# Performance work log

Measured on AMD Instinct MI355X. Metric: run time of the kernel, lower is better.

Reference implementation:

```python
import jax, jax.numpy as jnp
import numpy as np
from jax import lax

B, T_IN, T_AR = 512, 200, 200
H = 128
L = 2    # num_layers


def setup_inputs() -> dict:
    key = jax.random.key(0)
    k = jax.random.split(key, 8)
    s = 1.0 / np.sqrt(H)
    x = jax.random.normal(k[0], (B, T_IN, H), jnp.float32)
    lengths_in = jax.random.randint(k[1], (B,), T_IN // 2, T_IN + 1).astype(jnp.int32).at[0].set(T_IN)
    lengths_aureg = jax.random.randint(k[2], (B,), T_AR // 2, T_AR + 1).astype(jnp.int32).at[0].set(T_AR)
    mask_aureg = jnp.arange(T_AR)[None, :] < lengths_aureg[:, None]  # [B, T_ar] prefix mask
    W_ih = jax.random.uniform(k[3], (L, 4 * H, H), jnp.float32, -s, s)
    W_hh = jax.random.uniform(k[4], (L, 4 * H, H), jnp.float32, -s, s)
    b_ih = jax.random.uniform(k[5], (L, 4 * H), jnp.float32, -s, s)
    b_hh = jax.random.uniform(k[6], (L, 4 * H), jnp.float32, -s, s)
    return {"x": x, "lengths_in": lengths_in, "lengths_aureg": lengths_aureg,
            "mask_aureg": mask_aureg, "W_ih": W_ih, "W_hh": W_hh, "b_ih": b_ih, "b_hh": b_hh}


def _forward(x, lengths_in, mask_aureg, W_ih, W_hh, b_ih, b_hh):
    def cell_stack(x_t, h, c):
        # one LSTM time step through all layers. x_t: [B,H]; h,c: [L,B,H]
        inp = x_t
        hs, cs = [], []
        for l in range(L):
            z = inp @ W_ih[l].T + h[l] @ W_hh[l].T + (b_ih[l] + b_hh[l])
            i, f, g, o = jnp.split(z, 4, axis=-1)  # PyTorch gate order i,f,g,o
            c_new = jax.nn.sigmoid(f) * c[l] + jax.nn.sigmoid(i) * jnp.tanh(g)
            h_new = jax.nn.sigmoid(o) * jnp.tanh(c_new)
            hs.append(h_new)
            cs.append(c_new)
            inp = h_new
        return jnp.stack(hs), jnp.stack(cs)

    T_in = x.shape[1]
    mask_in = jnp.arange(T_in)[None, :] < lengths_in[:, None]  # [B, T_in]
    h0 = jnp.zeros((L, B, H), x.dtype)

    # Teacher-forcing pass == packed-sequence LSTM: states only advance where t < length,
    # padded output positions are zero (as pad_packed_sequence produces).
    def tf_step(carry, xs):
        h, c = carry
        x_t, m_t = xs  # [B,H], [B]
        h_new, c_new = cell_stack(x_t, h, c)
        m3 = m_t[None, :, None]
        h = jnp.where(m3, h_new, h)
        c = jnp.where(m3, c_new, c)
        out = jnp.where(m_t[:, None], h_new[-1], 0.0)
        return (h, c), out

    (h, c), outs_tf = lax.scan(tf_step, (h0, h0), (x.transpose(1, 0, 2), mask_in.T))
    outputs_teafo = outs_tf.transpose(1, 0, 2)  # [B, T_in, H]

    # input_aureg_init: last-layer hidden at each sequence's final real step
    x_init = h[-1]  # [B, H]

    def ar_step(carry, m_t):
        h, c, xp = carry
        h_new, c_new = cell_stack(xp, h, c)
        m3 = m_t[None, :, None]
        h = jnp.where(m3, h_new, h)
        c = jnp.where(m3, c_new, c)
        out = jnp.where(m_t[:, None], h_new[-1], 0.0)  # temp_output (zeros for inactive rows)
        return (h, c, out), out

    _, outs_ar = lax.scan(ar_step, (h, c, x_init), mask_aureg.T)
    outputs_aureg = outs_ar.transpose(1, 0, 2)  # [B, T_ar, H]
    return outputs_teafo, outputs_aureg


def reference(x, lengths_in, lengths_aureg, mask_aureg, W_ih, W_hh, b_ih, b_hh):
    return _forward(x, lengths_in, mask_aureg, W_ih, W_hh, b_ih, b_hh)
```

## Files before the change

### kernel.cpp

```cpp
#include <hip/hip_runtime.h>
#include <hip/hip_fp16.h>

typedef _Float16 half8 __attribute__((ext_vector_type(8)));
typedef _Float16 half4v __attribute__((ext_vector_type(4)));
typedef float f32x4 __attribute__((ext_vector_type(4)));

#define T_INS 200

constexpr int WI0O = 0;
constexpr int H0O  = 131072;
constexpr int H1O  = 139264;
constexpr int XTO  = 147456;
constexpr int BIO  = 155648;
constexpr int SMSZ = 159744;

#define OFF(b, k) (((((b) << 8) | ((k) << 1))) ^ (((b) & 7) << 4))

#define BARRIER() asm volatile("s_waitcnt lgkmcnt(0)\n\ts_barrier" ::: "memory")

__device__ __forceinline__ float sigm(float x) {
  return __builtin_amdgcn_rcpf(1.0f + __builtin_amdgcn_exp2f(-1.44269504f * x));
}
__device__ __forceinline__ float tanh_f(float x) {
  return 1.0f - 2.0f * __builtin_amdgcn_rcpf(1.0f + __builtin_amdgcn_exp2f(2.88539008f * x));
}
__device__ __forceinline__ half8 cvt_frag(const float* __restrict__ src) {
  f32x4 a = *(const f32x4*)src;
  f32x4 b = *(const f32x4*)(src + 4);
  half8 h;
  h[0] = (_Float16)a[0]; h[1] = (_Float16)a[1]; h[2] = (_Float16)a[2]; h[3] = (_Float16)a[3];
  h[4] = (_Float16)b[0]; h[5] = (_Float16)b[1]; h[6] = (_Float16)b[2]; h[7] = (_Float16)b[3];
  return h;
}
__device__ __forceinline__ int perm_row8(int w, int mt, int r) {
  return (r & 3) * 128 + w * 16 + (r >> 2) * 4 + mt;
}

__global__ __launch_bounds__(256) void pack_kernel(const float* __restrict__ W_ih,
                                                   const float* __restrict__ W_hh,
                                                   char* __restrict__ ws) {
  int gid = blockIdx.x * 256 + threadIdx.x;
  int G = gid >> 6, lane = gid & 63;
  int region = G >> 7, F = G & 127;
  int w = F >> 4, mt = (F >> 2) & 3, kf = F & 3;
  int row = perm_row8(w, mt, lane & 15);
  int k0 = kf * 32 + (lane >> 4) * 8;
  const float* src = (region == 0)
                         ? (W_ih + (size_t)(512 + row) * 128 + k0)
                         : (W_hh + (size_t)((region - 1) * 512 + row) * 128 + k0);
  *(half8*)(ws + (size_t)G * 1024 + lane * 16) = cvt_frag(src);
}

template <int PACKED>
__global__ __launch_bounds__(512, 2) void lstm_kernel(
    const float* __restrict__ x, const int* __restrict__ len_in,
    const int* __restrict__ len_ar, const float* __restrict__ W_ih,
    const float* __restrict__ W_hh, const float* __restrict__ b_ih,
    const float* __restrict__ b_hh, const char* __restrict__ ws,
    float* __restrict__ out) {
  __shared__ __attribute__((aligned(16))) char sm[SMSZ];
  float* biasS = (float*)(sm + BIO);

  const int tid = threadIdx.x;
  const int w = tid >> 6, lane = tid & 63;
  const int lb = lane & 15, lg = lane >> 4;
  const int k0b = lg * 8;
  const int u0 = w * 16 + lg * 4;
  const int batch = blockIdx.x * 16 + lb;
  const int Lin = len_in[batch];
  const int Lar = len_ar[batch];

  for (int j = 0; j < 16; ++j) {
    int pos = tid * 256 + j * 16;
    int F = pos >> 10, ln = (pos >> 4) & 63;
    int fw = F >> 4, fmt = (F >> 2) & 3, fkf = F & 3;
    int row = perm_row8(fw, fmt, ln & 15);
    int k0 = fkf * 32 + (ln >> 4) * 8;
    *(half8*)(sm + WI0O + pos) = cvt_frag(W_ih + (size_t)row * 128 + k0);
  }
  for (int i = tid; i < 1024; i += 512) {
    int l = i >> 9, rp = i & 511, u = rp >> 2, q = rp & 3;
    biasS[i] = b_ih[l * 512 + q * 128 + u] + b_hh[l * 512 + q * 128 + u];
  }
#pragma unroll
  for (int i = 0; i < 2; ++i)
    *(f32x4*)(sm + H0O + tid * 16 + i * 8192) = (f32x4){0.f, 0.f, 0.f, 0.f};
  const int xb = tid >> 5, xk4 = (tid & 31) * 4;
  {
    f32x4 v = *(const f32x4*)(x + ((size_t)(blockIdx.x * 16 + xb) * T_INS) * 128 + xk4);
    half4v hx;
    hx[0] = (_Float16)v[0]; hx[1] = (_Float16)v[1];
    hx[2] = (_Float16)v[2]; hx[3] = (_Float16)v[3];
    *(half4v*)(sm + XTO + OFF(xb, xk4)) = hx;
  }

  half8 whh0[4][4], whh1[4][4], wi1[4][4];
  if (PACKED) {
    const char* base = ws + (size_t)lane * 16;
#pragma unroll
    for (int mt = 0; mt < 4; ++mt)
#pragma unroll
      for (int kf = 0; kf < 4; ++kf) {
        int fo = (w * 16 + mt * 4 + kf) * 1024;
        wi1[mt][kf]  = *(const half8*)(base + fo);
        whh0[mt][kf] = *(const half8*)(base + 131072 + fo);
        whh1[mt][kf] = *(const half8*)(base + 262144 + fo);
      }
  } else {
#pragma unroll
    for (int mt = 0; mt < 4; ++mt)
#pragma unroll
      for (int kf = 0; kf < 4; ++kf) {
        int row = perm_row8(w, mt, lb);
        wi1[mt][kf]  = cvt_frag(W_ih + (size_t)(512 + row) * 128 + kf * 32 + k0b);
        whh0[mt][kf] = cvt_frag(W_hh + (size_t)row * 128 + kf * 32 + k0b);
        whh1[mt][kf] = cvt_frag(W_hh + (size_t)(512 + row) * 128 + kf * 32 + k0b);
      }
  }

  float c0[4], c1[4];
  half4v hp0v, hp1v;
#pragma unroll
  for (int i = 0; i < 4; ++i) {
    c0[i] = c1[i] = 0.f;
    hp0v[i] = (_Float16)0.f; hp1v[i] = (_Float16)0.f;
  }
  __syncthreads();

  const float* xptr = x + ((size_t)(blockIdx.x * 16 + xb) * T_INS + 1) * 128 + xk4;
  float* optr = out + (size_t)batch * 25600 + u0;
  const size_t obase_ar = 13107200ull + (size_t)batch * 25600 + u0;
  const char* wi0base = sm + WI0O + w * 16384 + lane * 16;

  for (int t = 0; t < 400; ++t) {
    const int p = t & 1;
    const bool doX = (t < 199);
    f32x4 xpre = (f32x4){0.f, 0.f, 0.f, 0.f};
    if (doX) { xpre = *(const f32x4*)xptr; xptr += 128; }
    const bool mk = (t < 200) ? (t < Lin) : ((t - 200) < Lar);

    f32x4 acc[4];
    {
      const char* sX = (t < 200) ? (sm + XTO + p * 4096) : (sm + H1O + p * 4096);
      const char* sH = sm + H0O + (p ^ 1) * 4096;
      half8 bf[4];
#pragma unroll
      for (int mt = 0; mt < 4; ++mt)
        acc[mt] = *(const f32x4*)(biasS + (u0 + mt) * 4);
#pragma unroll
      for (int kf = 0; kf < 4; ++kf)
        bf[kf] = *(const half8*)(sH + OFF(lb, kf * 32 + k0b));
#pragma unroll
      for (int kf = 0; kf < 4; ++kf)
#pragma unroll
        for (int mt = 0; mt < 4; ++mt)
          acc[mt] = __builtin_amdgcn_mfma_f32_16x16x32_f16(whh0[mt][kf], bf[kf],
                                                           acc[mt], 0, 0, 0);
#pragma unroll
      for (int kf = 0; kf < 4; ++kf)
        bf[kf] = *(const half8*)(sX + OFF(lb, kf * 32 + k0b));
#pragma unroll
      for (int kf = 0; kf < 4; ++kf)
#pragma unroll
        for (int mt = 0; mt < 4; ++mt) {
          half8 a = *(const half8*)(wi0base + (mt * 4 + kf) * 1024);
          acc[mt] = __builtin_amdgcn_mfma_f32_16x16x32_f16(a, bf[kf], acc[mt], 0, 0, 0);
        }
    }
    {
      _Float16 h4[4];
#pragma unroll
      for (int mt = 0; mt < 4; ++mt) {
        float si = sigm(acc[mt][0]);
        float sf = sigm(acc[mt][1]);
        float tg = tanh_f(acc[mt][2]);
        float so = sigm(acc[mt][3]);
        float cn = sf * c0[mt] + si * tg;
        float hn = so * tanh_f(cn);
        c0[mt] = mk ? cn : c0[mt];
        h4[mt] = (_Float16)hn;
      }
      hp0v = mk ? *(half4v*)h4 : hp0v;
      *(half4v*)(sm + H0O + p * 4096 + OFF(lb, u0)) = hp0v;
    }
    BARRIER();

    if (doX) {
      half4v hx;
      hx[0] = (_Float16)xpre[0]; hx[1] = (_Float16)xpre[1];
      hx[2] = (_Float16)xpre[2]; hx[3] = (_Float16)xpre[3];
      *(half4v*)(sm + XTO + (p ^ 1) * 4096 + OFF(xb, xk4)) = hx;
    }

    {
      const char* sX = sm + H0O + p * 4096;
      const char* sH = sm + H1O + p * 4096;
      half8 bf[4];
#pragma unroll
      for (int mt = 0; mt < 4; ++mt)
        acc[mt] = *(const f32x4*)(biasS + 512 + (u0 + mt) * 4);
#pragma unroll
      for (int kf = 0; kf < 4; ++kf)
        bf[kf] = *(const half8*)(sH + OFF(lb, kf * 32 + k0b));
#pragma unroll
      for (int kf = 0; kf < 4; ++kf)
#pragma unroll
        for (int mt = 0; mt < 4; ++mt)
          acc[mt] = __builtin_amdgcn_mfma_f32_16x16x32_f16(whh1[mt][kf], bf[kf],
                                                           acc[mt], 0, 0, 0);
#pragma unroll
      for (int kf = 0; kf < 4; ++kf)
        bf[kf] = *(const half8*)(sX + OFF(lb, kf * 32 + k0b));
#pragma unroll
      for (int kf = 0; kf < 4; ++kf)
#pragma unroll
        for (int mt = 0; mt < 4; ++mt)
          acc[mt] = __builtin_amdgcn_mfma_f32_16x16x32_f16(wi1[mt][kf], bf[kf],
                                                           acc[mt], 0, 0, 0);
    }
    {
      _Float16 h4[4];
      f32x4 vo;
#pragma unroll
      for (int mt = 0; mt < 4; ++mt) {
        float si = sigm(acc[mt][0]);
        float sf = sigm(acc[mt][1]);
        float tg = tanh_f(acc[mt][2]);
        float so = sigm(acc[mt][3]);
        float cn = sf * c1[mt] + si * tg;
        float hn = so * tanh_f(cn);
        c1[mt] = mk ? cn : c1[mt];
        h4[mt] = (_Float16)hn;
        vo[mt] = mk ? hn : 0.0f;
      }
      hp1v = mk ? *(half4v*)h4 : hp1v;
      *(half4v*)(sm + H1O + (p ^ 1) * 4096 + OFF(lb, u0)) = hp1v;
      *(f32x4*)optr = vo;
      optr += 128;
      if (t == 199) optr = out + obase_ar;
    }
    BARRIER();
  }
}

extern "C" void kernel_launch(void* const* d_in, const int* in_sizes, int n_in,
                              void* d_out, int out_size, void* d_ws, size_t ws_size,
                              hipStream_t stream) {
  (void)in_sizes; (void)n_in; (void)out_size;
  const float* x = (const float*)d_in[0];
  const int* len_in = (const int*)d_in[1];
  const int* len_ar = (const int*)d_in[2];
  const float* W_ih = (const float*)d_in[4];
  const float* W_hh = (const float*)d_in[5];
  const float* b_ih = (const float*)d_in[6];
  const float* b_hh = (const float*)d_in[7];
  float* out = (float*)d_out;
  char* ws = (char*)d_ws;

  if (ws_size >= (size_t)393216) {
    pack_kernel<<<dim3(96), dim3(256), 0, stream>>>(W_ih, W_hh, ws);
    lstm_kernel<1><<<dim3(32), dim3(512), 0, stream>>>(x, len_in, len_ar, W_ih,
                                                       W_hh, b_ih, b_hh, ws, out);
  } else {
    lstm_kernel<0><<<dim3(32), dim3(512), 0, stream>>>(x, len_in, len_ar, W_ih,
                                                       W_hh, b_ih, b_hh, ws, out);
  }
}
```

Baseline: 1.139 ms.

## Hoist layer-0 input projection into a parallel pre-GEMM and prefetch across barriers

Adds a zgemm kernel that computes the layer-0 input projection plus biases for all teacher-forcing timesteps in parallel and stores it to workspace. The recurrent kernel then loads these precomputed gate pre-activations instead of running the x-side MFMAs in the serial loop. The next operands (h fragments, bias, z values) are also issued before each barrier, with partial lgkmcnt waits and sched barriers, to overlap loads with the barrier. This needs about 200 MB of workspace and adds a global-memory load on the critical path at each step. If the workspace is too small it falls back to the old path.

```diff
diff --git a/kernel.cpp b/kernel.cpp
--- a/kernel.cpp
+++ b/kernel.cpp
@@ -14,9 +14,14 @@
 constexpr int BIO  = 155648;
 constexpr int SMSZ = 159744;
 
+constexpr size_t WSZ_PACK  = 524288;
+constexpr size_t Z0_BYTES  = 209715200ull;
+constexpr size_t WSZ_HOIST = WSZ_PACK + Z0_BYTES;
+
 #define OFF(b, k) (((((b) << 8) | ((k) << 1))) ^ (((b) & 7) << 4))
 
-#define BARRIER() asm volatile("s_waitcnt lgkmcnt(0)\n\ts_barrier" ::: "memory")
+#define BAR_K(n) asm volatile("s_waitcnt lgkmcnt(" #n ")\n\ts_barrier" ::: "memory")
+#define SCHED_FENCE() __builtin_amdgcn_sched_barrier(0)
 
 __device__ __forceinline__ float sigm(float x) {
   return __builtin_amdgcn_rcpf(1.0f + __builtin_amdgcn_exp2f(-1.44269504f * x));
@@ -45,13 +50,63 @@
   int w = F >> 4, mt = (F >> 2) & 3, kf = F & 3;
   int row = perm_row8(w, mt, lane & 15);
   int k0 = kf * 32 + (lane >> 4) * 8;
-  const float* src = (region == 0)
-                         ? (W_ih + (size_t)(512 + row) * 128 + k0)
-                         : (W_hh + (size_t)((region - 1) * 512 + row) * 128 + k0);
+  const float* src;
+  if (region == 0)      src = W_ih + (size_t)(512 + row) * 128 + k0;
+  else if (region == 3) src = W_ih + (size_t)row * 128 + k0;
+  else                  src = W_hh + (size_t)((region - 1) * 512 + row) * 128 + k0;
   *(half8*)(ws + (size_t)G * 1024 + lane * 16) = cvt_frag(src);
 }
 
-template <int PACKED>
+__global__ __launch_bounds__(512) void zgemm_kernel(const float* __restrict__ x,
+                                                    const float* __restrict__ b_ih,
+                                                    const float* __restrict__ b_hh,
+                                                    char* __restrict__ ws) {
+  __shared__ __attribute__((aligned(16))) char sx[4096];
+  const int tid = threadIdx.x;
+  const int w = tid >> 6, lane = tid & 63;
+  const int lb = lane & 15, lg = lane >> 4;
+  const int k0b = lg * 8;
+  const int u0 = w * 16 + lg * 4;
+  const int t = blockIdx.x >> 5, bg = blockIdx.x & 31;
+
+  {
+    int b = tid >> 5, k4 = (tid & 31) * 4;
+    f32x4 v = *(const f32x4*)(x + ((size_t)(bg * 16 + b) * T_INS + t) * 128 + k4);
+    half4v hx;
+    hx[0] = (_Float16)v[0]; hx[1] = (_Float16)v[1];
+    hx[2] = (_Float16)v[2]; hx[3] = (_Float16)v[3];
+    *(half4v*)(sx + OFF(b, k4)) = hx;
+  }
+  __syncthreads();
+
+  f32x4 acc[4];
+#pragma unroll
+  for (int mt = 0; mt < 4; ++mt)
+#pragma unroll
+    for (int q = 0; q < 4; ++q)
+      acc[mt][q] = b_ih[q * 128 + u0 + mt] + b_hh[q * 128 + u0 + mt];
+
+  half8 bf[4];
+#pragma unroll
+  for (int kf = 0; kf < 4; ++kf)
+    bf[kf] = *(const half8*)(sx + OFF(lb, kf * 32 + k0b));
+
+  const char* wbase = ws + 393216 + (size_t)lane * 16;
+#pragma unroll
+  for (int kf = 0; kf < 4; ++kf)
+#pragma unroll
+    for (int mt = 0; mt < 4; ++mt) {
+      half8 a = *(const half8*)(wbase + (w * 16 + mt * 4 + kf) * 1024);
+      acc[mt] = __builtin_amdgcn_mfma_f32_16x16x32_f16(a, bf[kf], acc[mt], 0, 0, 0);
+    }
+
+  char* zp = ws + WSZ_PACK + ((size_t)blockIdx.x * 8 + w) * 4096 + lane * 16;
+#pragma unroll
+  for (int mt = 0; mt < 4; ++mt)
+    *(f32x4*)(zp + mt * 1024) = acc[mt];
+}
+
+template <int PACKED, int HOIST>
 __global__ __launch_bounds__(512, 2) void lstm_kernel(
     const float* __restrict__ x, const int* __restrict__ len_in,
     const int* __restrict__ len_ar, const float* __restrict__ W_ih,
@@ -85,8 +140,9 @@
 #pragma unroll
   for (int i = 0; i < 2; ++i)
     *(f32x4*)(sm + H0O + tid * 16 + i * 8192) = (f32x4){0.f, 0.f, 0.f, 0.f};
+
   const int xb = tid >> 5, xk4 = (tid & 31) * 4;
-  {
+  if (!HOIST) {
     f32x4 v = *(const f32x4*)(x + ((size_t)(blockIdx.x * 16 + xb) * T_INS) * 128 + xk4);
     half4v hx;
     hx[0] = (_Float16)v[0]; hx[1] = (_Float16)v[1];
@@ -131,31 +187,37 @@
   float* optr = out + (size_t)batch * 25600 + u0;
   const size_t obase_ar = 13107200ull + (size_t)batch * 25600 + u0;
   const char* wi0base = sm + WI0O + w * 16384 + lane * 16;
+  const char* zp = ws + WSZ_PACK + ((size_t)(blockIdx.x * 8 + w)) * 4096 + lane * 16;
+
+  f32x4 acc[4];
+  half8 bf[4];
+  if (HOIST) {
+#pragma unroll
+    for (int mt = 0; mt < 4; ++mt) acc[mt] = *(const f32x4*)(zp + mt * 1024);
+  } else {
+#pragma unroll
+    for (int mt = 0; mt < 4; ++mt) acc[mt] = *(const f32x4*)(biasS + (u0 + mt) * 4);
+  }
+#pragma unroll
+  for (int kf = 0; kf < 4; ++kf)
+    bf[kf] = *(const half8*)(sm + H0O + 4096 + OFF(lb, kf * 32 + k0b));
 
   for (int t = 0; t < 400; ++t) {
     const int p = t & 1;
-    const bool doX = (t < 199);
+    const bool tf = (t < 200);
+    const bool mk = tf ? (t < Lin) : ((t - 200) < Lar);
+
     f32x4 xpre = (f32x4){0.f, 0.f, 0.f, 0.f};
-    if (doX) { xpre = *(const f32x4*)xptr; xptr += 128; }
-    const bool mk = (t < 200) ? (t < Lin) : ((t - 200) < Lar);
-
-    f32x4 acc[4];
-    {
-      const char* sX = (t < 200) ? (sm + XTO + p * 4096) : (sm + H1O + p * 4096);
-      const char* sH = sm + H0O + (p ^ 1) * 4096;
-      half8 bf[4];
+    if (!HOIST && t < 199) { xpre = *(const f32x4*)xptr; xptr += 128; }
+
+#pragma unroll
+    for (int kf = 0; kf < 4; ++kf)
 #pragma unroll
       for (int mt = 0; mt < 4; ++mt)
-        acc[mt] = *(const f32x4*)(biasS + (u0 + mt) * 4);
-#pragma unroll
-      for (int kf = 0; kf < 4; ++kf)
-        bf[kf] = *(const half8*)(sH + OFF(lb, kf * 32 + k0b));
-#pragma unroll
-      for (int kf = 0; kf < 4; ++kf)
-#pragma unroll
-        for (int mt = 0; mt < 4; ++mt)
-          acc[mt] = __builtin_amdgcn_mfma_f32_16x16x32_f16(whh0[mt][kf], bf[kf],
-                                                           acc[mt], 0, 0, 0);
+        acc[mt] = __builtin_amdgcn_mfma_f32_16x16x32_f16(whh0[mt][kf], bf[kf],
+                                                         acc[mt], 0, 0, 0);
+    if (!HOIST || !tf) {
+      const char* sX = tf ? (sm + XTO + p * 4096) : (sm + H1O + p * 4096);
 #pragma unroll
       for (int kf = 0; kf < 4; ++kf)
         bf[kf] = *(const half8*)(sX + OFF(lb, kf * 32 + k0b));
@@ -183,41 +245,40 @@
       hp0v = mk ? *(half4v*)h4 : hp0v;
       *(half4v*)(sm + H0O + p * 4096 + OFF(lb, u0)) = hp0v;
     }
-    BARRIER();
-
-    if (doX) {
+    SCHED_FENCE();
+    if (tf) {
+#pragma unroll
+      for (int kf = 0; kf < 4; ++kf)
+        bf[kf] = *(const half8*)(sm + H1O + p * 4096 + OFF(lb, kf * 32 + k0b));
+    }
+#pragma unroll
+    for (int mt = 0; mt < 4; ++mt)
+      acc[mt] = *(const f32x4*)(biasS + 512 + (u0 + mt) * 4);
+    SCHED_FENCE();
+    if (tf) BAR_K(8); else BAR_K(4);
+
+    if (!HOIST && t < 199) {
       half4v hx;
       hx[0] = (_Float16)xpre[0]; hx[1] = (_Float16)xpre[1];
       hx[2] = (_Float16)xpre[2]; hx[3] = (_Float16)xpre[3];
       *(half4v*)(sm + XTO + (p ^ 1) * 4096 + OFF(xb, xk4)) = hx;
     }
 
-    {
-      const char* sX = sm + H0O + p * 4096;
-      const char* sH = sm + H1O + p * 4096;
-      half8 bf[4];
+#pragma unroll
+    for (int kf = 0; kf < 4; ++kf)
 #pragma unroll
       for (int mt = 0; mt < 4; ++mt)
-        acc[mt] = *(const f32x4*)(biasS + 512 + (u0 + mt) * 4);
-#pragma unroll
-      for (int kf = 0; kf < 4; ++kf)
-        bf[kf] = *(const half8*)(sH + OFF(lb, kf * 32 + k0b));
-#pragma unroll
-      for (int kf = 0; kf < 4; ++kf)
-#pragma unroll
-        for (int mt = 0; mt < 4; ++mt)
-          acc[mt] = __builtin_amdgcn_mfma_f32_16x16x32_f16(whh1[mt][kf], bf[kf],
-                                                           acc[mt], 0, 0, 0);
-#pragma unroll
-      for (int kf = 0; kf < 4; ++kf)
-        bf[kf] = *(const half8*)(sX + OFF(lb, kf * 32 + k0b));
-#pragma unroll
-      for (int kf = 0; kf < 4; ++kf)
-#pragma unroll
-        for (int mt = 0; mt < 4; ++mt)
-          acc[mt] = __builtin_amdgcn_mfma_f32_16x16x32_f16(wi1[mt][kf], bf[kf],
-                                                           acc[mt], 0, 0, 0);
-    }
+        acc[mt] = __builtin_amdgcn_mfma_f32_16x16x32_f16(whh1[mt][kf], bf[kf],
+                                                         acc[mt], 0, 0, 0);
+#pragma unroll
+    for (int kf = 0; kf < 4; ++kf)
+      bf[kf] = *(const half8*)(sm + H0O + p * 4096 + OFF(lb, kf * 32 + k0b));
+#pragma unroll
+    for (int kf = 0; kf < 4; ++kf)
+#pragma unroll
+      for (int mt = 0; mt < 4; ++mt)
+        acc[mt] = __builtin_amdgcn_mfma_f32_16x16x32_f16(wi1[mt][kf], bf[kf],
+                                                         acc[mt], 0, 0, 0);
     {
       _Float16 h4[4];
       f32x4 vo;
@@ -239,7 +300,19 @@
       optr += 128;
       if (t == 199) optr = out + obase_ar;
     }
-    BARRIER();
+    SCHED_FENCE();
+    if (HOIST && t + 1 < 200) {
+      zp += 1048576;
+#pragma unroll
+      for (int mt = 0; mt < 4; ++mt) acc[mt] = *(const f32x4*)(zp + mt * 1024);
+      SCHED_FENCE();
+      BAR_K(0);
+    } else {
+#pragma unroll
+      for (int mt = 0; mt < 4; ++mt) acc[mt] = *(const f32x4*)(biasS + (u0 + mt) * 4);
+      SCHED_FENCE();
+      BAR_K(4);
+    }
   }
 }
 
@@ -257,12 +330,19 @@
   float* out = (float*)d_out;
   char* ws = (char*)d_ws;
 
-  if (ws_size >= (size_t)393216) {
-    pack_kernel<<<dim3(96), dim3(256), 0, stream>>>(W_ih, W_hh, ws);
-    lstm_kernel<1><<<dim3(32), dim3(512), 0, stream>>>(x, len_in, len_ar, W_ih,
-                                                       W_hh, b_ih, b_hh, ws, out);
-  } else {
-    lstm_kernel<0><<<dim3(32), dim3(512), 0, stream>>>(x, len_in, len_ar, W_ih,
-                                                       W_hh, b_ih, b_hh, ws, out);
-  }
-}
+  const bool packed = ws_size >= WSZ_PACK;
+  const bool hoist  = ws_size >= WSZ_HOIST;
+
+  if (packed) pack_kernel<<<dim3(128), dim3(256), 0, stream>>>(W_ih, W_hh, ws);
+  if (hoist)  zgemm_kernel<<<dim3(6400), dim3(512), 0, stream>>>(x, b_ih, b_hh, ws);
+
+  if (hoist)
+    lstm_kernel<1, 1><<<dim3(32), dim3(512), 0, stream>>>(x, len_in, len_ar, W_ih,
+                                                          W_hh, b_ih, b_hh, ws, out);
+  else if (packed)
+    lstm_kernel<1, 0><<<dim3(32), dim3(512), 0, stream>>>(x, len_in, len_ar, W_ih,
+                                                          W_hh, b_ih, b_hh, ws, out);
+  else
+    lstm_kernel<0, 0><<<dim3(32), dim3(512), 0, stream>>>(x, len_in, len_ar, W_ih,
+                                                          W_hh, b_ih, b_hh, ws, out);
+}
```

Result: slower. 1.305 ms (+14.6%).

## Skew layer pipeline in teacher-forcing phase and prescale gate weights

Applied to the files above, without the earlier changes.

During teacher forcing, layer 1 at step t now runs alongside layer 0 at step t+1, so each step needs one barrier instead of two. Barriers wait with lgkmcnt(N) so that bias preloads stay in flight across them. Weights and biases are prescaled in the pack kernel by the exp2 constants, removing a multiply from each gate activation. W_ih layer 0 is also packed in global memory, so the kernel copies it into shared memory without converting it. The autoregressive phase keeps its serial dependency but is restructured to overlap loads, and the extra fp16 rounding of the prescaled weights may slightly change precision.

```diff
diff --git a/kernel.cpp b/kernel.cpp
--- a/kernel.cpp
+++ b/kernel.cpp
@@ -14,9 +14,12 @@
 constexpr int BIO  = 155648;
 constexpr int SMSZ = 159744;
 
+constexpr size_t WSZ_PACK = 524288;
+
 #define OFF(b, k) (((((b) << 8) | ((k) << 1))) ^ (((b) & 7) << 4))
 
-#define BARRIER() asm volatile("s_waitcnt lgkmcnt(0)\n\ts_barrier" ::: "memory")
+#define BAR_K(n) asm volatile("s_waitcnt lgkmcnt(" #n ")\n\ts_barrier" ::: "memory")
+#define SCHED_FENCE() __builtin_amdgcn_sched_barrier(0)
 
 __device__ __forceinline__ float sigm(float x) {
   return __builtin_amdgcn_rcpf(1.0f + __builtin_amdgcn_exp2f(-1.44269504f * x));
@@ -32,8 +35,35 @@
   h[4] = (_Float16)b[0]; h[5] = (_Float16)b[1]; h[6] = (_Float16)b[2]; h[7] = (_Float16)b[3];
   return h;
 }
+__device__ __forceinline__ half8 cvt_frag_s(const float* __restrict__ src, float s) {
+  f32x4 a = *(const f32x4*)src;
+  f32x4 b = *(const f32x4*)(src + 4);
+  half8 h;
+  h[0] = (_Float16)(s * a[0]); h[1] = (_Float16)(s * a[1]);
+  h[2] = (_Float16)(s * a[2]); h[3] = (_Float16)(s * a[3]);
+  h[4] = (_Float16)(s * b[0]); h[5] = (_Float16)(s * b[1]);
+  h[6] = (_Float16)(s * b[2]); h[7] = (_Float16)(s * b[3]);
+  return h;
+}
 __device__ __forceinline__ int perm_row8(int w, int mt, int r) {
   return (r & 3) * 128 + w * 16 + (r >> 2) * 4 + mt;
+}
+
+template <int SCALED>
+__device__ __forceinline__ float gates(const f32x4 a, float& c, bool mk) {
+  float si, sf, tg, so;
+  if (SCALED) {
+    si = __builtin_amdgcn_rcpf(1.0f + __builtin_amdgcn_exp2f(a[0]));
+    sf = __builtin_amdgcn_rcpf(1.0f + __builtin_amdgcn_exp2f(a[1]));
+    tg = 1.0f - 2.0f * __builtin_amdgcn_rcpf(1.0f + __builtin_amdgcn_exp2f(a[2]));
+    so = __builtin_amdgcn_rcpf(1.0f + __builtin_amdgcn_exp2f(a[3]));
+  } else {
+    si = sigm(a[0]); sf = sigm(a[1]); tg = tanh_f(a[2]); so = sigm(a[3]);
+  }
+  float cn = sf * c + si * tg;
+  float hn = so * tanh_f(cn);
+  c = mk ? cn : c;
+  return hn;
 }
 
 __global__ __launch_bounds__(256) void pack_kernel(const float* __restrict__ W_ih,
@@ -43,13 +73,33 @@
   int G = gid >> 6, lane = gid & 63;
   int region = G >> 7, F = G & 127;
   int w = F >> 4, mt = (F >> 2) & 3, kf = F & 3;
-  int row = perm_row8(w, mt, lane & 15);
+  int r = lane & 15;
+  int row = perm_row8(w, mt, r);
   int k0 = kf * 32 + (lane >> 4) * 8;
-  const float* src = (region == 0)
-                         ? (W_ih + (size_t)(512 + row) * 128 + k0)
-                         : (W_hh + (size_t)((region - 1) * 512 + row) * 128 + k0);
-  *(half8*)(ws + (size_t)G * 1024 + lane * 16) = cvt_frag(src);
-}
+  float s = ((r & 3) == 2) ? 2.88539008f : -1.44269504f;
+  const float* src;
+  if (region == 0)      src = W_ih + (size_t)(512 + row) * 128 + k0;
+  else if (region == 3) src = W_ih + (size_t)row * 128 + k0;
+  else                  src = W_hh + (size_t)((region - 1) * 512 + row) * 128 + k0;
+  *(half8*)(ws + (size_t)G * 1024 + lane * 16) = cvt_frag_s(src, s);
+}
+
+#define READ_BF(BF, BASE)                                                     \
+  _Pragma("unroll") for (int kf = 0; kf < 4; ++kf)                            \
+      BF[kf] = *(const half8*)((BASE) + OFF(lb, kf * 32 + k0b));
+
+#define MFMA4x4(ACC, WREG, BF)                                                \
+  _Pragma("unroll") for (int kf = 0; kf < 4; ++kf)                            \
+      _Pragma("unroll") for (int mt = 0; mt < 4; ++mt)                        \
+          ACC[mt] = __builtin_amdgcn_mfma_f32_16x16x32_f16(WREG[mt][kf],      \
+                                                           BF[kf], ACC[mt], 0, 0, 0);
+
+#define MFMA_WI0(ACC, BF)                                                     \
+  _Pragma("unroll") for (int kf = 0; kf < 4; ++kf)                            \
+      _Pragma("unroll") for (int mt = 0; mt < 4; ++mt) {                      \
+        half8 a_ = *(const half8*)(wi0base + (mt * 4 + kf) * 1024);           \
+        ACC[mt] = __builtin_amdgcn_mfma_f32_16x16x32_f16(a_, BF[kf], ACC[mt], 0, 0, 0); \
+      }
 
 template <int PACKED>
 __global__ __launch_bounds__(512, 2) void lstm_kernel(
@@ -70,28 +120,39 @@
   const int Lin = len_in[batch];
   const int Lar = len_ar[batch];
 
-  for (int j = 0; j < 16; ++j) {
-    int pos = tid * 256 + j * 16;
-    int F = pos >> 10, ln = (pos >> 4) & 63;
-    int fw = F >> 4, fmt = (F >> 2) & 3, fkf = F & 3;
-    int row = perm_row8(fw, fmt, ln & 15);
-    int k0 = fkf * 32 + (ln >> 4) * 8;
-    *(half8*)(sm + WI0O + pos) = cvt_frag(W_ih + (size_t)row * 128 + k0);
+  if (PACKED) {
+    for (int j = 0; j < 16; ++j) {
+      int pos = j * 8192 + tid * 16;
+      *(half8*)(sm + WI0O + pos) = *(const half8*)(ws + 393216 + pos);
+    }
+  } else {
+    for (int j = 0; j < 16; ++j) {
+      int pos = tid * 256 + j * 16;
+      int F = pos >> 10, ln = (pos >> 4) & 63;
+      int fw = F >> 4, fmt = (F >> 2) & 3, fkf = F & 3;
+      int row = perm_row8(fw, fmt, ln & 15);
+      int k0 = fkf * 32 + (ln >> 4) * 8;
+      *(half8*)(sm + WI0O + pos) = cvt_frag(W_ih + (size_t)row * 128 + k0);
+    }
   }
   for (int i = tid; i < 1024; i += 512) {
     int l = i >> 9, rp = i & 511, u = rp >> 2, q = rp & 3;
-    biasS[i] = b_ih[l * 512 + q * 128 + u] + b_hh[l * 512 + q * 128 + u];
+    float s = PACKED ? ((q == 2) ? 2.88539008f : -1.44269504f) : 1.0f;
+    biasS[i] = s * (b_ih[l * 512 + q * 128 + u] + b_hh[l * 512 + q * 128 + u]);
   }
 #pragma unroll
   for (int i = 0; i < 2; ++i)
     *(f32x4*)(sm + H0O + tid * 16 + i * 8192) = (f32x4){0.f, 0.f, 0.f, 0.f};
   const int xb = tid >> 5, xk4 = (tid & 31) * 4;
   {
-    f32x4 v = *(const f32x4*)(x + ((size_t)(blockIdx.x * 16 + xb) * T_INS) * 128 + xk4);
-    half4v hx;
-    hx[0] = (_Float16)v[0]; hx[1] = (_Float16)v[1];
-    hx[2] = (_Float16)v[2]; hx[3] = (_Float16)v[3];
-    *(half4v*)(sm + XTO + OFF(xb, xk4)) = hx;
+    const float* xp0 = x + ((size_t)(blockIdx.x * 16 + xb) * T_INS) * 128 + xk4;
+    f32x4 v0 = *(const f32x4*)xp0;
+    f32x4 v1 = *(const f32x4*)(xp0 + 128);
+    half4v h0x, h1x;
+#pragma unroll
+    for (int i = 0; i < 4; ++i) { h0x[i] = (_Float16)v0[i]; h1x[i] = (_Float16)v1[i]; }
+    *(half4v*)(sm + XTO + OFF(xb, xk4)) = h0x;
+    *(half4v*)(sm + XTO + 4096 + OFF(xb, xk4)) = h1x;
   }
 
   half8 whh0[4][4], whh1[4][4], wi1[4][4];
@@ -127,119 +188,146 @@
   }
   __syncthreads();
 
-  const float* xptr = x + ((size_t)(blockIdx.x * 16 + xb) * T_INS + 1) * 128 + xk4;
+  const char* wi0base = sm + WI0O + w * 16384 + lane * 16;
+  const float* xptr = x + ((size_t)(blockIdx.x * 16 + xb) * T_INS + 2) * 128 + xk4;
   float* optr = out + (size_t)batch * 25600 + u0;
   const size_t obase_ar = 13107200ull + (size_t)batch * 25600 + u0;
-  const char* wi0base = sm + WI0O + w * 16384 + lane * 16;
-
-  for (int t = 0; t < 400; ++t) {
+
+  f32x4 acc0[4], acc1[4];
+  half8 bfA[4], bfB[4];
+
+  {
+    READ_BF(bfB, sm + XTO);
+#pragma unroll
+    for (int mt = 0; mt < 4; ++mt) acc0[mt] = *(const f32x4*)(biasS + (u0 + mt) * 4);
+    MFMA_WI0(acc0, bfB);
+    const bool mk0 = (0 < Lin);
+    half4v h4;
+#pragma unroll
+    for (int mt = 0; mt < 4; ++mt) h4[mt] = (_Float16)gates<PACKED>(acc0[mt], c0[mt], mk0);
+    hp0v = mk0 ? h4 : hp0v;
+    *(half4v*)(sm + H0O + OFF(lb, u0)) = hp0v;
+    SCHED_FENCE();
+#pragma unroll
+    for (int mt = 0; mt < 4; ++mt) acc1[mt] = *(const f32x4*)(biasS + 512 + (u0 + mt) * 4);
+#pragma unroll
+    for (int mt = 0; mt < 4; ++mt) acc0[mt] = *(const f32x4*)(biasS + (u0 + mt) * 4);
+    SCHED_FENCE();
+    BAR_K(8);
+  }
+
+  for (int t = 0; t < 199; ++t) {
     const int p = t & 1;
-    const bool doX = (t < 199);
-    f32x4 xpre = (f32x4){0.f, 0.f, 0.f, 0.f};
+    const bool doX = (t < 198);
+    f32x4 xpre;
     if (doX) { xpre = *(const f32x4*)xptr; xptr += 128; }
-    const bool mk = (t < 200) ? (t < Lin) : ((t - 200) < Lar);
-
-    f32x4 acc[4];
+    const bool mk1 = (t < Lin), mk0 = ((t + 1) < Lin);
+
+    READ_BF(bfB, sm + H1O + (p ^ 1) * 4096);
+    READ_BF(bfA, sm + H0O + p * 4096);
+    MFMA4x4(acc1, whh1, bfB);
+    MFMA4x4(acc0, whh0, bfA);
+    MFMA4x4(acc1, wi1, bfA);
+    READ_BF(bfB, sm + XTO + (p ^ 1) * 4096);
+    MFMA_WI0(acc0, bfB);
+
     {
-      const char* sX = (t < 200) ? (sm + XTO + p * 4096) : (sm + H1O + p * 4096);
-      const char* sH = sm + H0O + (p ^ 1) * 4096;
-      half8 bf[4];
-#pragma unroll
-      for (int mt = 0; mt < 4; ++mt)
-        acc[mt] = *(const f32x4*)(biasS + (u0 + mt) * 4);
-#pragma unroll
-      for (int kf = 0; kf < 4; ++kf)
-        bf[kf] = *(const half8*)(sH + OFF(lb, kf * 32 + k0b));
-#pragma unroll
-      for (int kf = 0; kf < 4; ++kf)
-#pragma unroll
-        for (int mt = 0; mt < 4; ++mt)
-          acc[mt] = __builtin_amdgcn_mfma_f32_16x16x32_f16(whh0[mt][kf], bf[kf],
-                                                           acc[mt], 0, 0, 0);
-#pragma unroll
-      for (int kf = 0; kf < 4; ++kf)
-        bf[kf] = *(const half8*)(sX + OFF(lb, kf * 32 + k0b));
-#pragma unroll
-      for (int kf = 0; kf < 4; ++kf)
-#pragma unroll
-        for (int mt = 0; mt < 4; ++mt) {
-          half8 a = *(const half8*)(wi0base + (mt * 4 + kf) * 1024);
-          acc[mt] = __builtin_amdgcn_mfma_f32_16x16x32_f16(a, bf[kf], acc[mt], 0, 0, 0);
-        }
+      half4v h4; f32x4 vo;
+#pragma unroll
+      for (int mt = 0; mt < 4; ++mt) {
+        float hn = gates<PACKED>(acc1[mt], c1[mt], mk1);
+        h4[mt] = (_Float16)hn;
+        vo[mt] = mk1 ? hn : 0.0f;
+      }
+      hp1v = mk1 ? h4 : hp1v;
+      *(half4v*)(sm + H1O + p * 4096 + OFF(lb, u0)) = hp1v;
+      *(f32x4*)optr = vo; optr += 128;
     }
     {
-      _Float16 h4[4];
-#pragma unroll
-      for (int mt = 0; mt < 4; ++mt) {
-        float si = sigm(acc[mt][0]);
-        float sf = sigm(acc[mt][1]);
-        float tg = tanh_f(acc[mt][2]);
-        float so = sigm(acc[mt][3]);
-        float cn = sf * c0[mt] + si * tg;
-        float hn = so * tanh_f(cn);
-        c0[mt] = mk ? cn : c0[mt];
-        h4[mt] = (_Float16)hn;
-      }
-      hp0v = mk ? *(half4v*)h4 : hp0v;
-      *(half4v*)(sm + H0O + p * 4096 + OFF(lb, u0)) = hp0v;
-    }
-    BARRIER();
-
+      half4v h4;
+#pragma unroll
+      for (int mt = 0; mt < 4; ++mt) h4[mt] = (_Float16)gates<PACKED>(acc0[mt], c0[mt], mk0);
+      hp0v = mk0 ? h4 : hp0v;
+      *(half4v*)(sm + H0O + (p ^ 1) * 4096 + OFF(lb, u0)) = hp0v;
+    }
     if (doX) {
       half4v hx;
-      hx[0] = (_Float16)xpre[0]; hx[1] = (_Float16)xpre[1];
-      hx[2] = (_Float16)xpre[2]; hx[3] = (_Float16)xpre[3];
-      *(half4v*)(sm + XTO + (p ^ 1) * 4096 + OFF(xb, xk4)) = hx;
-    }
-
+#pragma unroll
+      for (int i = 0; i < 4; ++i) hx[i] = (_Float16)xpre[i];
+      *(half4v*)(sm + XTO + p * 4096 + OFF(xb, xk4)) = hx;
+    }
+    SCHED_FENCE();
+#pragma unroll
+    for (int mt = 0; mt < 4; ++mt) acc1[mt] = *(const f32x4*)(biasS + 512 + (u0 + mt) * 4);
+#pragma unroll
+    for (int mt = 0; mt < 4; ++mt) acc0[mt] = *(const f32x4*)(biasS + (u0 + mt) * 4);
+    SCHED_FENCE();
+    BAR_K(8);
+  }
+
+  {
+    READ_BF(bfB, sm + H1O);
+    READ_BF(bfA, sm + H0O + 4096);
+    MFMA4x4(acc1, whh1, bfB);
+    MFMA4x4(acc1, wi1, bfA);
+    BAR_K(0);
+    const bool mk1 = (199 < Lin);
+    half4v h4; f32x4 vo;
+#pragma unroll
+    for (int mt = 0; mt < 4; ++mt) {
+      float hn = gates<PACKED>(acc1[mt], c1[mt], mk1);
+      h4[mt] = (_Float16)hn;
+      vo[mt] = mk1 ? hn : 0.0f;
+    }
+    hp1v = mk1 ? h4 : hp1v;
+    *(half4v*)(sm + H1O + OFF(lb, u0)) = hp1v;
+    *(f32x4*)optr = vo;
+    optr = out + obase_ar;
+    SCHED_FENCE();
+#pragma unroll
+    for (int mt = 0; mt < 4; ++mt) acc0[mt] = *(const f32x4*)(biasS + (u0 + mt) * 4);
+    SCHED_FENCE();
+    BAR_K(4);
+  }
+
+  for (int t = 200; t < 400; ++t) {
+    const int p = t & 1;
+    const bool mk = (t - 200) < Lar;
+    MFMA4x4(acc0, whh0, bfA);
+    READ_BF(bfB, sm + H1O + p * 4096);
+    MFMA_WI0(acc0, bfB);
     {
-      const char* sX = sm + H0O + p * 4096;
-      const char* sH = sm + H1O + p * 4096;
-      half8 bf[4];
-#pragma unroll
-      for (int mt = 0; mt < 4; ++mt)
-        acc[mt] = *(const f32x4*)(biasS + 512 + (u0 + mt) * 4);
-#pragma unroll
-      for (int kf = 0; kf < 4; ++kf)
-        bf[kf] = *(const half8*)(sH + OFF(lb, kf * 32 + k0b));
-#pragma unroll
-      for (int kf = 0; kf < 4; ++kf)
-#pragma unroll
-        for (int mt = 0; mt < 4; ++mt)
-          acc[mt] = __builtin_amdgcn_mfma_f32_16x16x32_f16(whh1[mt][kf], bf[kf],
-                                                           acc[mt], 0, 0, 0);
-#pragma unroll
-      for (int kf = 0; kf < 4; ++kf)
-        bf[kf] = *(const half8*)(sX + OFF(lb, kf * 32 + k0b));
-#pragma unroll
-      for (int kf = 0; kf < 4; ++kf)
-#pragma unroll
-        for (int mt = 0; mt < 4; ++mt)
-          acc[mt] = __builtin_amdgcn_mfma_f32_16x16x32_f16(wi1[mt][kf], bf[kf],
-                                                           acc[mt], 0, 0, 0);
-    }
+      half4v h4;
+#pragma unroll
+      for (int mt = 0; mt < 4; ++mt) h4[mt] = (_Float16)gates<PACKED>(acc0[mt], c0[mt], mk);
+      hp0v = mk ? h4 : hp0v;
+      *(half4v*)(sm + H0O + p * 4096 + OFF(lb, u0)) = hp0v;
+    }
+    SCHED_FENCE();
+#pragma unroll
+    for (int mt = 0; mt < 4; ++mt) acc1[mt] = *(const f32x4*)(biasS + 512 + (u0 + mt) * 4);
+    SCHED_FENCE();
+    BAR_K(4);
+    MFMA4x4(acc1, whh1, bfB);
+    READ_BF(bfA, sm + H0O + p * 4096);
+    MFMA4x4(acc1, wi1, bfA);
     {
-      _Float16 h4[4];
-      f32x4 vo;
+      half4v h4; f32x4 vo;
 #pragma unroll
       for (int mt = 0; mt < 4; ++mt) {
-        float si = sigm(acc[mt][0]);
-        float sf = sigm(acc[mt][1]);
-        float tg = tanh_f(acc[mt][2]);
-        float so = sigm(acc[mt][3]);
-        float cn = sf * c1[mt] + si * tg;
-        float hn = so * tanh_f(cn);
-        c1[mt] = mk ? cn : c1[mt];
+        float hn = gates<PACKED>(acc1[mt], c1[mt], mk);
         h4[mt] = (_Float16)hn;
         vo[mt] = mk ? hn : 0.0f;
       }
-      hp1v = mk ? *(half4v*)h4 : hp1v;
+      hp1v = mk ? h4 : hp1v;
       *(half4v*)(sm + H1O + (p ^ 1) * 4096 + OFF(lb, u0)) = hp1v;
-      *(f32x4*)optr = vo;
-      optr += 128;
-      if (t == 199) optr = out + obase_ar;
-    }
-    BARRIER();
+      *(f32x4*)optr = vo; optr += 128;
+    }
+    SCHED_FENCE();
+#pragma unroll
+    for (int mt = 0; mt < 4; ++mt) acc0[mt] = *(const f32x4*)(biasS + (u0 + mt) * 4);
+    SCHED_FENCE();
+    BAR_K(4);
   }
 }
 
@@ -257,8 +345,8 @@
   float* out = (float*)d_out;
   char* ws = (char*)d_ws;
 
-  if (ws_size >= (size_t)393216) {
-    pack_kernel<<<dim3(96), dim3(256), 0, stream>>>(W_ih, W_hh, ws);
+  if (ws_size >= WSZ_PACK) {
+    pack_kernel<<<dim3(128), dim3(256), 0, stream>>>(W_ih, W_hh, ws);
     lstm_kernel<1><<<dim3(32), dim3(512), 0, stream>>>(x, len_in, len_ar, W_ih,
                                                        W_hh, b_ih, b_hh, ws, out);
   } else {
```

After: 1.405 ms. +23.4%, slower.
